# Kernel optimization log

Hardware: AMD Instinct MI355X
Metric: run time of the kernel (lower is better)

## Reference

```python
import jax, jax.numpy as jnp
import numpy as np

N, T, V = 64, 256, 10000          # batch, caption length, vocab
D_FEAT, W_DIM, H_DIM = 1280, 256, 512  # mobilenet feat, wordvec, hidden
NULL = 0                           # word_to_idx['<NULL>'] == ignore_index


def setup_inputs() -> dict:
    key = jax.random.key(0)
    ks = jax.random.split(key, 9)
    feat = jax.random.normal(ks[0], (N, D_FEAT), jnp.float32)
    captions = jax.random.randint(ks[1], (N, T), 0, V)
    # parameters (init mirrors the torch module: randn/sqrt(fan_in), zero bias)
    W_proj = jax.random.normal(ks[2], (D_FEAT, H_DIM), jnp.float32) / np.sqrt(D_FEAT).astype(np.float32)
    b_proj = jnp.zeros((H_DIM,), jnp.float32)
    W_embed = jax.random.normal(ks[3], (V, W_DIM), jnp.float32) / np.sqrt(V).astype(np.float32)
    Wx = jax.random.normal(ks[4], (W_DIM, H_DIM), jnp.float32) / np.sqrt(W_DIM).astype(np.float32)
    Wh = jax.random.normal(ks[5], (H_DIM, H_DIM), jnp.float32) / np.sqrt(H_DIM).astype(np.float32)
    b = jnp.zeros((H_DIM,), jnp.float32)
    W_out = jax.random.normal(ks[6], (H_DIM, V), jnp.float32) / np.sqrt(H_DIM).astype(np.float32)
    b_out = jnp.zeros((V,), jnp.float32)
    return {"feat": feat, "W_proj": W_proj, "b_proj": b_proj,
            "W_embed": W_embed, "Wx": Wx, "Wh": Wh, "b": b,
            "W_out": W_out, "b_out": b_out, "captions": captions}


def reference(feat, W_proj, b_proj, W_embed, Wx, Wh, b, W_out, b_out, captions):
    cap_in = captions[:, :-1]   # (N, T-1) inputs
    cap_out = captions[:, 1:]   # (N, T-1) targets

    h0 = feat @ W_proj + b_proj                 # (N, H)
    emb = W_embed[cap_in]                       # (N, T-1, W)
    # input-to-hidden projection has no recurrent dependency: batch it
    xW = jnp.einsum('ntw,wh->nth', emb, Wx) + b # (N, T-1, H)

    def step(h, xw_t):                           # xw_t: (N, H)
        h_next = jnp.tanh(xw_t + h @ Wh)
        return h_next, h_next

    _, hs = jax.lax.scan(step, h0, jnp.swapaxes(xW, 0, 1))
    hs = jnp.swapaxes(hs, 0, 1)                 # (N, T-1, H)

    scores = jnp.einsum('nth,hv->ntv', hs, W_out) + b_out  # (N, T-1, V)
    logp = jax.nn.log_softmax(scores, axis=-1)
    picked = jnp.take_along_axis(logp, cap_out[..., None], axis=-1)[..., 0]
    mask = (cap_out != NULL).astype(scores.dtype)
    # cross_entropy(..., reduction='sum', ignore_index=NULL) / N
    loss = -(picked * mask).sum() / N
    return loss
```

## Files before the change

### kernel.cpp

```cpp
#include <hip/hip_runtime.h>

#define NS 64
#define TT 256
#define TS 255
#define VV 10000
#define DF 1280
#define WD 256
#define HD 512
#define RTOT (TS*NS)
#define RPAD 16384

#define TANH_SCALE 2.8853900817779268f
#define LOG2E 1.4426950408889634f

typedef __attribute__((ext_vector_type(4))) float f32x4;
typedef __attribute__((ext_vector_type(8))) short s16x8;
typedef __attribute__((ext_vector_type(4))) unsigned int u32x4;
typedef __attribute__((ext_vector_type(8))) int i32x8;

__device__ __forceinline__ unsigned short f2bf(float f){
  unsigned u; __builtin_memcpy(&u, &f, 4);
  u += 0x7FFFu + ((u >> 16) & 1u);
  return (unsigned short)(u >> 16);
}
__device__ __forceinline__ float bf2f(unsigned short h){
  unsigned u = ((unsigned)h) << 16; float f; __builtin_memcpy(&f, &u, 4); return f;
}
__device__ __forceinline__ unsigned char f2fp8(float f){
  int p = __builtin_amdgcn_cvt_pk_fp8_f32(f, f, 0, false);
  return (unsigned char)(p & 0xFF);
}
__device__ __forceinline__ float dot4_fp8(unsigned int a, unsigned int b){
  float d;
  d  = __builtin_amdgcn_cvt_f32_fp8(a, 0) * __builtin_amdgcn_cvt_f32_fp8(b, 0);
  d += __builtin_amdgcn_cvt_f32_fp8(a, 1) * __builtin_amdgcn_cvt_f32_fp8(b, 1);
  d += __builtin_amdgcn_cvt_f32_fp8(a, 2) * __builtin_amdgcn_cvt_f32_fp8(b, 2);
  d += __builtin_amdgcn_cvt_f32_fp8(a, 3) * __builtin_amdgcn_cvt_f32_fp8(b, 3);
  return d;
}
__device__ __forceinline__ f32x4 mfma128(i32x8 a, i32x8 b, f32x4 c){
  return __builtin_amdgcn_mfma_scale_f32_16x16x128_f8f6f4(a, b, c, 0, 0, 0, 127, 0, 127);
}

__device__ __forceinline__ void transpose_cvt_blk(const float* __restrict__ src,
    unsigned char* __restrict__ dst, int R, int C, int bx, int by, int fp8, int tid){
  __shared__ float tile[32][33];
  int r0 = bx*32, c0 = by*32;
  int tr = tid >> 5, tc = tid & 31;
  #pragma unroll
  for(int p=0;p<4;p++){
    int r = r0 + tr + p*8, c = c0 + tc;
    tile[tr + p*8][tc] = (r < R && c < C) ? src[r*C + c] : 0.f;
  }
  __syncthreads();
  #pragma unroll
  for(int p=0;p<4;p++){
    int oc = c0 + tr + p*8;
    int orow = r0 + tc;
    if(oc < C && orow < R){
      float v = tile[tc][tr + p*8];
      if(fp8) dst[oc*R + orow] = f2fp8(v);
      else ((unsigned short*)dst)[oc*R + orow] = f2bf(v);
    }
  }
}

__global__ __launch_bounds__(256) void k_conv(const float* __restrict__ W_proj,
    const float* __restrict__ Wx, const float* __restrict__ Wh,
    const float* __restrict__ W_out, const float* __restrict__ feat,
    const float* __restrict__ W_embed,
    unsigned short* __restrict__ WprojT, unsigned short* __restrict__ WxT,
    unsigned char* __restrict__ Wh8S, unsigned char* __restrict__ WoutT,
    unsigned short* __restrict__ featb, unsigned short* __restrict__ Wembb,
    float* __restrict__ out0){
  int b = blockIdx.x, tid = threadIdx.x;
  if(b == 0 && tid == 0) out0[0] = 0.f;
  if(b < 640){
    transpose_cvt_blk(W_proj, (unsigned char*)WprojT, 1280, 512, b%40, b/40, 0, tid);
  } else if(b < 768){
    int bb = b - 640;
    transpose_cvt_blk(Wx, (unsigned char*)WxT, 256, 512, bb%8, bb/8, 0, tid);
  } else if(b < 1792){
    int i = (b-768)*256 + tid;
    int blk = i>>11;
    int w = blk>>4, ct = (blk>>2)&3, kq = blk&3;
    int lane = (i>>5)&63, ib = i&31;
    int q = lane>>4, rrr = lane&15;
    int k = kq*128 + q*32 + ib;
    int j = w*64 + ct*16 + rrr;
    Wh8S[i] = f2fp8(Wh[k*HD + j] * TANH_SCALE);
  } else if(b < 6800){
    int bb = b - 1792;
    transpose_cvt_blk(W_out, WoutT, 512, 10000, bb%16, bb/16, 1, tid);
  } else if(b < 6840){
    int i = ((b-6800)*256 + tid)*8;
    f32x4 v0 = *(const f32x4*)(feat + i);
    f32x4 v1 = *(const f32x4*)(feat + i + 4);
    s16x8 o;
    #pragma unroll
    for(int j=0;j<4;j++){ o[j] = (short)f2bf(v0[j]); o[j+4] = (short)f2bf(v1[j]); }
    *(s16x8*)(featb + i) = o;
  } else {
    int i = ((b-6840)*256 + tid)*8;
    f32x4 v0 = *(const f32x4*)(W_embed + i);
    f32x4 v1 = *(const f32x4*)(W_embed + i + 4);
    s16x8 o;
    #pragma unroll
    for(int j=0;j<4;j++){ o[j] = (short)f2bf(v0[j]); o[j+4] = (short)f2bf(v1[j]); }
    *(s16x8*)(Wembb + i) = o;
  }
}

__global__ __launch_bounds__(256) void k_h0(const unsigned short* __restrict__ featb,
    const unsigned short* __restrict__ WprojT, const float* __restrict__ b_proj,
    unsigned short* __restrict__ h0b){
  __shared__ unsigned short Al[64*264];
  __shared__ unsigned short Bl[64*264];
  int tid = threadIdx.x, cb = blockIdx.x;
  int w = tid>>6, lane = tid&63, q = lane>>4, rr = lane&15;
  f32x4 acc[4];
  #pragma unroll
  for(int i=0;i<4;i++){ acc[i][0]=0.f; acc[i][1]=0.f; acc[i][2]=0.f; acc[i][3]=0.f; }
  for(int kb=0; kb<5; kb++){
    {
      int row = tid >> 2, part = tid & 3;
      const u32x4* s = (const u32x4*)(featb + row*DF + kb*256 + part*64);
      u32x4* d = (u32x4*)(Al + row*264 + part*64);
      #pragma unroll
      for(int i=0;i<8;i++) d[i] = s[i];
    }
    {
      int row = tid >> 2, part = tid & 3;
      int j = cb*64 + row;
      const u32x4* s = (const u32x4*)(WprojT + j*DF + kb*256 + part*64);
      u32x4* d = (u32x4*)(Bl + row*264 + part*64);
      #pragma unroll
      for(int i=0;i<8;i++) d[i] = s[i];
    }
    __syncthreads();
    #pragma unroll
    for(int kc=0;kc<8;kc++){
      s16x8 a = *(const s16x8*)(Al + (w*16 + rr)*264 + kc*32 + q*8);
      #pragma unroll
      for(int tc=0;tc<4;tc++){
        s16x8 bb = *(const s16x8*)(Bl + (tc*16 + rr)*264 + kc*32 + q*8);
        acc[tc] = __builtin_amdgcn_mfma_f32_16x16x32_bf16(a, bb, acc[tc], 0, 0, 0);
      }
    }
    __syncthreads();
  }
  #pragma unroll
  for(int tc=0;tc<4;tc++){
    #pragma unroll
    for(int reg=0;reg<4;reg++){
      int n = w*16 + q*4 + reg;
      int j = cb*64 + tc*16 + rr;
      h0b[n*HD + j] = f2bf(acc[tc][reg] + b_proj[j]);
    }
  }
}

__global__ __launch_bounds__(256) void k_xw(const unsigned short* __restrict__ Wembb,
    const unsigned short* __restrict__ WxT, const float* __restrict__ bvec,
    const int* __restrict__ captions, unsigned short* __restrict__ xWk){
  __shared__ unsigned short Al[64*264];
  __shared__ unsigned short Bl[64*264];
  int tid = threadIdx.x, cb = blockIdx.x, t = blockIdx.y;
  int w = tid>>6, lane = tid&63, q = lane>>4, rr = lane&15;
  {
    int row = tid >> 2, part = tid & 3;
    int idx = captions[row*TT + t];
    const u32x4* s = (const u32x4*)(Wembb + idx*WD + part*64);
    u32x4* d = (u32x4*)(Al + row*264 + part*64);
    #pragma unroll
    for(int i=0;i<8;i++) d[i] = s[i];
  }
  {
    int row = tid >> 2, part = tid & 3;
    int j = cb*64 + row;
    const u32x4* s = (const u32x4*)(WxT + j*WD + part*64);
    u32x4* d = (u32x4*)(Bl + row*264 + part*64);
    #pragma unroll
    for(int i=0;i<8;i++) d[i] = s[i];
  }
  __syncthreads();
  f32x4 acc[4];
  #pragma unroll
  for(int i=0;i<4;i++){ acc[i][0]=0.f; acc[i][1]=0.f; acc[i][2]=0.f; acc[i][3]=0.f; }
  #pragma unroll
  for(int kc=0;kc<8;kc++){
    s16x8 a = *(const s16x8*)(Al + (w*16 + rr)*264 + kc*32 + q*8);
    #pragma unroll
    for(int tc=0;tc<4;tc++){
      s16x8 bb = *(const s16x8*)(Bl + (tc*16 + rr)*264 + kc*32 + q*8);
      acc[tc] = __builtin_amdgcn_mfma_f32_16x16x32_bf16(a, bb, acc[tc], 0, 0, 0);
    }
  }
  #pragma unroll
  for(int tc=0;tc<4;tc++){
    int j = cb*64 + tc*16 + rr;
    float bo = bvec[j];
    unsigned short st[4];
    #pragma unroll
    for(int reg=0;reg<4;reg++)
      st[reg] = f2bf((acc[tc][reg] + bo) * TANH_SCALE);
    size_t f = (((size_t)t*4 + w)*8 + cb)*1024 + q*256 + rr*16 + tc*4;
    unsigned long v; __builtin_memcpy(&v, st, 8);
    *(unsigned long*)(xWk + f) = v;
  }
}

__global__ __launch_bounds__(512, 2) void k_rnn(const unsigned short* __restrict__ h0b,
    const unsigned char* __restrict__ Wh8S, const unsigned short* __restrict__ xWk,
    unsigned char* __restrict__ hs8){
  __shared__ unsigned char hbuf[2][16*560];
  int tid = threadIdx.x, w = tid>>6, lane = tid&63, q = lane>>4, rr = lane&15;
  int n0 = blockIdx.x * 16;
  int j0 = w * 64;
  i32x8 wb[16];
  #pragma unroll
  for(int ct=0;ct<4;ct++)
    #pragma unroll
    for(int kq=0;kq<4;kq++)
      wb[ct*4+kq] = *(const i32x8*)(Wh8S + (size_t)((w*4+ct)*4+kq)*2048 + lane*32);
  {
    int s = tid>>5, c0 = (tid&31)*16;
    #pragma unroll
    for(int i=0;i<16;i++)
      hbuf[0][s*560 + c0 + i] = f2fp8(bf2f(h0b[(n0+s)*HD + c0 + i]));
  }
  __syncthreads();
  int scp = tid>>5, scc = (tid&31)*16;
  const unsigned short* xp = xWk + (((size_t)blockIdx.x)*8 + w)*1024 + q*256 + rr*16;
  unsigned short xs[16];
  *(u32x4*)(xs)   = *(const u32x4*)(xp);
  *(u32x4*)(xs+8) = *(const u32x4*)(xp+8);
  for(int t=0; t<TS; t++){
    const unsigned char* hb = hbuf[t&1];
    unsigned char*       hn = hbuf[(t&1)^1];
    if(t)
      *(u32x4*)(hs8 + (size_t)((t-1)*NS + n0 + scp)*HD + scc) = *(const u32x4*)(hb + scp*560 + scc);
    f32x4 acc[4];
    #pragma unroll
    for(int ct=0;ct<4;ct++)
      #pragma unroll
      for(int reg=0;reg<4;reg++)
        acc[ct][reg] = bf2f(xs[ct*4+reg]);
    unsigned short xn[16];
    *(u32x4*)(xn)   = *(const u32x4*)(xp + 32768);
    *(u32x4*)(xn+8) = *(const u32x4*)(xp + 32768 + 8);
    i32x8 af[4];
    #pragma unroll
    for(int kq=0;kq<4;kq++)
      af[kq] = *(const i32x8*)(hb + rr*560 + kq*128 + q*32);
    #pragma unroll
    for(int ct=0;ct<4;ct++)
      #pragma unroll
      for(int kq=0;kq<4;kq++)
        acc[ct] = mfma128(af[kq], wb[ct*4+kq], acc[ct]);
    #pragma unroll
    for(int ct=0;ct<4;ct++){
      int j = j0 + ct*16 + rr;
      #pragma unroll
      for(int reg=0;reg<4;reg++){
        int nl = q*4 + reg;
        float e2 = __builtin_amdgcn_exp2f(acc[ct][reg]);
        float h = __builtin_fmaf(-2.f, __builtin_amdgcn_rcpf(e2 + 1.f), 1.f);
        hn[nl*560 + j] = f2fp8(h);
      }
    }
    __syncthreads();
    xp += 32768;
    *(u32x4*)(xs)   = *(u32x4*)(xn);
    *(u32x4*)(xs+8) = *(u32x4*)(xn+8);
  }
  *(u32x4*)(hs8 + (size_t)((TS-1)*NS + n0 + scp)*HD + scc) = *(const u32x4*)(hbuf[TS&1] + scp*560 + scc);
}

__global__ __launch_bounds__(256, 2) void k_scores(const unsigned char* __restrict__ hs8,
    const unsigned char* __restrict__ WoutT, const float* __restrict__ b_out,
    float* __restrict__ partial_s){
  __shared__ unsigned char Bl[128*528];
  __shared__ float sred[2][128];
  int tid = threadIdx.x;
  int chunk = blockIdx.x, rb = blockIdx.y;
  int w = tid>>6, lane = tid&63, q = lane>>4, rr = lane&15;
  int wi = w>>1, wj = w&1;
  long af[4][16];
  #pragma unroll
  for(int tr=0;tr<4;tr++)
    #pragma unroll
    for(int kc=0;kc<16;kc++){
      int row = rb*128 + wi*64 + tr*16 + rr;
      af[tr][kc] = *(const long*)(hs8 + (size_t)row*HD + kc*32 + q*8);
    }
  float sacc[16];
  #pragma unroll
  for(int i=0;i<16;i++) sacc[i]=0.f;
  int vc0 = chunk*2500, vc1 = vc0 + 2500;
  for(int vt=0; vt<20; vt++){
    int vbase = vc0 + vt*128;
    {
      int v = tid>>1, half = tid&1;
      int vg = vbase + v; if(vg > VV-1) vg = VV-1;
      const u32x4* s = (const u32x4*)(WoutT + (size_t)vg*HD + half*256);
      u32x4* d = (u32x4*)(Bl + v*528 + half*256);
      #pragma unroll
      for(int i=0;i<16;i++) d[i] = s[i];
    }
    __syncthreads();
    f32x4 acc[4][4];
    #pragma unroll
    for(int a=0;a<4;a++)
      #pragma unroll
      for(int b=0;b<4;b++){ acc[a][b][0]=0.f; acc[a][b][1]=0.f; acc[a][b][2]=0.f; acc[a][b][3]=0.f; }
    #pragma unroll
    for(int kc=0;kc<16;kc++){
      long bf[4];
      #pragma unroll
      for(int tc=0;tc<4;tc++)
        bf[tc] = *(const long*)(Bl + (wj*64 + tc*16 + rr)*528 + kc*32 + q*8);
      #pragma unroll
      for(int tr=0;tr<4;tr++)
        #pragma unroll
        for(int tc=0;tc<4;tc++)
          acc[tr][tc] = __builtin_amdgcn_mfma_f32_16x16x32_fp8_fp8(af[tr][kc], bf[tc], acc[tr][tc], 0, 0, 0);
    }
    #pragma unroll
    for(int tc=0;tc<4;tc++){
      int vg = vbase + wj*64 + tc*16 + rr;
      bool vok = vg < vc1;
      float boc = vok ? b_out[vg]*LOG2E : 0.f;
      #pragma unroll
      for(int tr=0;tr<4;tr++)
        #pragma unroll
        for(int reg=0;reg<4;reg++){
          float ex = __builtin_amdgcn_exp2f(__builtin_fmaf(acc[tr][tc][reg], LOG2E, boc));
          if(vok) sacc[tr*4+reg] += ex;
        }
    }
    __syncthreads();
  }
  #pragma unroll
  for(int i=0;i<16;i++){
    float v = sacc[i];
    v += __shfl_xor(v, 1, 64);
    v += __shfl_xor(v, 2, 64);
    v += __shfl_xor(v, 4, 64);
    v += __shfl_xor(v, 8, 64);
    sacc[i] = v;
  }
  if(rr == 0){
    #pragma unroll
    for(int tr=0;tr<4;tr++)
      #pragma unroll
      for(int reg=0;reg<4;reg++)
        sred[wj][wi*64 + tr*16 + q*4 + reg] = sacc[tr*4+reg];
  }
  __syncthreads();
  if(tid < 128){
    int row = rb*128 + tid;
    if(row < RTOT) partial_s[row*4 + chunk] = sred[0][tid] + sred[1][tid];
  }
}

__global__ __launch_bounds__(256) void k_pickedloss(const unsigned char* __restrict__ hs8,
    const unsigned char* __restrict__ WoutT, const float* __restrict__ b_out,
    const int* __restrict__ captions, const float* __restrict__ partial_s,
    float* __restrict__ out){
  int tid = threadIdx.x;
  int w = tid>>6, lane = tid&63;
  int R = blockIdx.x*4 + w;
  int t = R >> 6, n = R & 63;
  int y = captions[n*TT + t + 1];
  const unsigned int* hp = (const unsigned int*)(hs8 + (size_t)R*HD + lane*8);
  const unsigned int* wp = (const unsigned int*)(WoutT + (size_t)y*HD + lane*8);
  unsigned int hv0 = hp[0], hv1 = hp[1], wv0 = wp[0], wv1 = wp[1];
  float d = dot4_fp8(hv0, wv0) + dot4_fp8(hv1, wv1);
  d += __shfl_xor(d, 1, 64);
  d += __shfl_xor(d, 2, 64);
  d += __shfl_xor(d, 4, 64);
  d += __shfl_xor(d, 8, 64);
  d += __shfl_xor(d, 16, 64);
  d += __shfl_xor(d, 32, 64);
  __shared__ float red[4];
  if(lane == 0){
    float contrib = 0.f;
    if(y != 0){
      float picked = d + b_out[y];
      float s = partial_s[R*4] + partial_s[R*4+1] + partial_s[R*4+2] + partial_s[R*4+3];
      contrib = __logf(s) - picked;
    }
    red[w] = contrib;
  }
  __syncthreads();
  if(tid == 0){
    float v = (red[0]+red[1]+red[2]+red[3]) * (1.0f/64.0f);
    atomicAdd(out, v);
  }
}

extern "C" void kernel_launch(void* const* d_in, const int* in_sizes, int n_in,
                              void* d_out, int out_size, void* d_ws, size_t ws_size,
                              hipStream_t stream) {
  const float* feat    = (const float*)d_in[0];
  const float* W_proj  = (const float*)d_in[1];
  const float* b_proj  = (const float*)d_in[2];
  const float* W_embed = (const float*)d_in[3];
  const float* Wx      = (const float*)d_in[4];
  const float* Wh      = (const float*)d_in[5];
  const float* bvec    = (const float*)d_in[6];
  const float* W_out   = (const float*)d_in[7];
  const float* b_out   = (const float*)d_in[8];
  const int*   captions= (const int*)d_in[9];

  char* p = (char*)d_ws;
  unsigned short* WprojT = (unsigned short*)p;  p += 512*1280*2;
  unsigned short* WxT    = (unsigned short*)p;  p += 512*256*2;
  unsigned char*  Wh8S   = (unsigned char*)p;   p += 512*512;
  unsigned char*  WoutT  = (unsigned char*)p;   p += 10000*512;
  unsigned short* Wembb  = (unsigned short*)p;  p += 10000*256*2;
  unsigned short* featb  = (unsigned short*)p;  p += 64*1280*2;
  unsigned short* h0b    = (unsigned short*)p;  p += 64*512*2;
  unsigned short* xWk    = (unsigned short*)p;  p += TS*64*512*2;
  unsigned char*  hs8    = (unsigned char*)p;   p += RPAD*512;
  float* partial_s       = (float*)p;           p += RTOT*4*4;
  if((size_t)(p - (char*)d_ws) > ws_size) return;

  k_conv<<<8090, 256, 0, stream>>>(W_proj, Wx, Wh, W_out, feat, W_embed,
                                   WprojT, WxT, Wh8S, WoutT, featb, Wembb,
                                   (float*)d_out);
  k_h0<<<8, 256, 0, stream>>>(featb, WprojT, b_proj, h0b);
  k_xw<<<dim3(8, TS), 256, 0, stream>>>(Wembb, WxT, bvec, captions, xWk);
  k_rnn<<<4, 512, 0, stream>>>(h0b, Wh8S, xWk, hs8);
  k_scores<<<dim3(4, 128), 256, 0, stream>>>(hs8, WoutT, b_out, partial_s);
  k_pickedloss<<<4080, 256, 0, stream>>>(hs8, WoutT, b_out, captions, partial_s, (float*)d_out);
}
```

Measured before the change: 642.5 us.

## Stage xW stores through LDS, pack fp8 hidden writes, remap score block order

```diff
diff --git a/kernel.cpp b/kernel.cpp
--- a/kernel.cpp
+++ b/kernel.cpp
@@ -196,17 +196,25 @@
       acc[tc] = __builtin_amdgcn_mfma_f32_16x16x32_bf16(a, bb, acc[tc], 0, 0, 0);
     }
   }
+  __syncthreads();
+  unsigned short* sx = (unsigned short*)Al;
   #pragma unroll
   for(int tc=0;tc<4;tc++){
     int j = cb*64 + tc*16 + rr;
     float bo = bvec[j];
-    unsigned short st[4];
     #pragma unroll
     for(int reg=0;reg<4;reg++)
-      st[reg] = f2bf((acc[tc][reg] + bo) * TANH_SCALE);
-    size_t f = (((size_t)t*4 + w)*8 + cb)*1024 + q*256 + rr*16 + tc*4;
-    unsigned long v; __builtin_memcpy(&v, st, 8);
-    *(unsigned long*)(xWk + f) = v;
+      sx[w*1024 + (rr>>2)*256 + (q*4+reg)*16 + tc*4 + (rr&3)]
+        = f2bf((acc[tc][reg] + bo) * TANH_SCALE);
+  }
+  __syncthreads();
+  {
+    int o = tid*16;
+    int blk = o >> 10, inner = o & 1023;
+    unsigned short* dst = xWk + (((size_t)t*4 + blk)*8 + cb)*1024 + inner;
+    const u32x4* s = (const u32x4*)(sx + o);
+    *(u32x4*)(dst)     = s[0];
+    *(u32x4*)(dst + 8) = s[1];
   }
 }
 
@@ -257,17 +265,18 @@
     for(int ct=0;ct<4;ct++)
       #pragma unroll
       for(int kq=0;kq<4;kq++)
-        acc[ct] = mfma128(af[kq], wb[ct*4+kq], acc[ct]);
+        acc[ct] = mfma128(wb[ct*4+kq], af[kq], acc[ct]);
     #pragma unroll
     for(int ct=0;ct<4;ct++){
-      int j = j0 + ct*16 + rr;
+      float h[4];
       #pragma unroll
       for(int reg=0;reg<4;reg++){
-        int nl = q*4 + reg;
         float e2 = __builtin_amdgcn_exp2f(acc[ct][reg]);
-        float h = __builtin_fmaf(-2.f, __builtin_amdgcn_rcpf(e2 + 1.f), 1.f);
-        hn[nl*560 + j] = f2fp8(h);
+        h[reg] = __builtin_fmaf(-2.f, __builtin_amdgcn_rcpf(e2 + 1.f), 1.f);
       }
+      int pk = __builtin_amdgcn_cvt_pk_fp8_f32(h[0], h[1], 0, false);
+      pk     = __builtin_amdgcn_cvt_pk_fp8_f32(h[2], h[3], pk, true);
+      *(unsigned int*)(hn + rr*560 + j0 + ct*16 + q*4) = (unsigned)pk;
     }
     __syncthreads();
     xp += 32768;
@@ -283,7 +292,10 @@
   __shared__ unsigned char Bl[128*528];
   __shared__ float sred[2][128];
   int tid = threadIdx.x;
-  int chunk = blockIdx.x, rb = blockIdx.y;
+  int bid = blockIdx.x;
+  int c = bid & 7;
+  int chunk = c & 3;
+  int rb = (bid >> 3) + ((c >> 2) << 6);
   int w = tid>>6, lane = tid&63, q = lane>>4, rr = lane&15;
   int wi = w>>1, wj = w&1;
   long af[4][16];
@@ -433,6 +445,6 @@
   k_h0<<<8, 256, 0, stream>>>(featb, WprojT, b_proj, h0b);
   k_xw<<<dim3(8, TS), 256, 0, stream>>>(Wembb, WxT, bvec, captions, xWk);
   k_rnn<<<4, 512, 0, stream>>>(h0b, Wh8S, xWk, hs8);
-  k_scores<<<dim3(4, 128), 256, 0, stream>>>(hs8, WoutT, b_out, partial_s);
+  k_scores<<<512, 256, 0, stream>>>(hs8, WoutT, b_out, partial_s);
   k_pickedloss<<<4080, 256, 0, stream>>>(hs8, WoutT, b_out, captions, partial_s, (float*)d_out);
 }
```

New measurement: 603.6 us. 1.06x faster.
